# Kernel optimization log

Hardware: AMD Instinct MI355X
Metric: run time of the kernel (lower is better)

Reference implementation:

```python
import jax, jax.numpy as jnp
import numpy as np

B, N, C = 2048, 4096, 1024
UNITS, RANK = 4096, 512


def _orth(key, shape):
    a = jax.random.normal(key, shape, dtype=jnp.float32)
    q, r = jnp.linalg.qr(a if shape[0] >= shape[1] else a.T)
    q = q * jnp.sign(jnp.diagonal(r))[None, :]
    return q if shape[0] >= shape[1] else q.T


def setup_inputs() -> dict:
    key = jax.random.key(0)
    k1, k2, k3, k4, k5, k6 = jax.random.split(key, 6)
    inputs = jax.random.normal(k1, (B, N), dtype=jnp.float32)
    context = jax.random.normal(k2, (B, C), dtype=jnp.float32)
    U = _orth(k3, (N, RANK))
    V = _orth(k4, (UNITS, RANK))
    W = _orth(k5, (C, RANK))
    # SingularValueInitializer stand-in: positive values scaled like glorot singular values
    S = jnp.abs(jax.random.normal(k6, (RANK,), dtype=jnp.float32)) * jnp.sqrt(2.0 / (N + UNITS))
    bias = jnp.zeros((UNITS,), dtype=jnp.float32)
    return {"inputs": inputs, "context": context, "U": U, "S": S, "V": V, "W": W, "bias": bias}


def reference(inputs, context, U, S, V, W, bias):
    # s_b = S + context @ W  -> per-batch singular values [B, R]
    s = S[None, :] + context @ W
    # Original: kernel_b = U diag(s_b) V^T; out_b = x_b @ kernel_b.
    # Associativity: out = ((x @ U) * s) @ V^T  -- identical math, no [B,N,M] intermediate.
    xu = inputs @ U                      # [B, R]
    out = (xu * s) @ V.T                 # [B, UNITS]
    out = out + bias[None, :]
    return jax.nn.relu(out)
```

## Files before the change

### kernel.cpp

```cpp
#include <hip/hip_runtime.h>
#include <hip/hip_bf16.h>

typedef __attribute__((ext_vector_type(8))) __bf16 bf16x8;
typedef __attribute__((ext_vector_type(4))) float f32x4;
typedef __attribute__((ext_vector_type(8))) unsigned short ushort8;
typedef __attribute__((ext_vector_type(4))) unsigned short ushort4v;

__device__ __forceinline__ unsigned short f2bf(float f) {
  unsigned u = __builtin_bit_cast(unsigned, f);
  u += 0x7FFFu + ((u >> 16) & 1u);
  return (unsigned short)(u >> 16);
}

__device__ __forceinline__ void gload_lds16(const void* g, void* l) {
  __builtin_amdgcn_global_load_lds(
      (const __attribute__((address_space(1))) void*)g,
      (__attribute__((address_space(3))) void*)l, 16, 0, 0);
}

__device__ __forceinline__ void barrier_fence() {
  __builtin_amdgcn_s_barrier();
  asm volatile("" ::: "memory");
}

template <int N>
__device__ __forceinline__ void waitvm() {
  if constexpr (N == 0)      asm volatile("s_waitcnt vmcnt(0)" ::: "memory");
  else if constexpr (N == 8) asm volatile("s_waitcnt vmcnt(8)" ::: "memory");
}

__global__ __launch_bounds__(256) void prep_kernel(
    const float* __restrict__ U, unsigned short* __restrict__ Ut,
    const float* __restrict__ W, unsigned short* __restrict__ Wt,
    const float* __restrict__ V, unsigned short* __restrict__ Vb) {
  __shared__ float tile[32][33];
  const int b = blockIdx.x;
  const int tid = threadIdx.x;
  if (b < 2560) {
    const float* src;
    unsigned short* dst;
    int rows, cols, bx, by;
    if (b < 2048) {
      src = U; dst = Ut; rows = 4096; cols = 512;
      bx = (b & 15) * 32; by = (b >> 4) * 32;
    } else {
      int bb = b - 2048;
      src = W; dst = Wt; rows = 1024; cols = 512;
      bx = (bb & 15) * 32; by = (bb >> 4) * 32;
    }
    const int tx = tid & 31, ty = tid >> 5;
    for (int i = ty; i < 32; i += 8)
      tile[i][tx] = src[(size_t)(by + i) * cols + bx + tx];
    __syncthreads();
    for (int i = ty; i < 32; i += 8)
      dst[(size_t)(bx + i) * rows + by + tx] = f2bf(tile[tx][i]);
  } else {
    const size_t i = (size_t)(b - 2560) * 256 + tid;
    const float4* s4 = reinterpret_cast<const float4*>(V) + 2 * i;
    float4 a = s4[0], c = s4[1];
    ushort8 o;
    o[0] = f2bf(a.x); o[1] = f2bf(a.y); o[2] = f2bf(a.z); o[3] = f2bf(a.w);
    o[4] = f2bf(c.x); o[5] = f2bf(c.y); o[6] = f2bf(c.z); o[7] = f2bf(c.w);
    *(reinterpret_cast<ushort8*>(Vb) + i) = o;
  }
}

template <int FM, int FN, int EPI, int DEPTH>
__device__ __forceinline__ void gemm_core(
    const unsigned short* __restrict__ A, const unsigned short* __restrict__ Bt,
    int N, int lda, int kchunk, const float* __restrict__ e0,
    float* __restrict__ outf, int nwg, int bid) {
  constexpr int BM = 32 * FM, BN = 32 * FN, BK = 64;
  constexpr int AI = FM, BI = FN;
  constexpr int ISS = AI + BI;
  __shared__ unsigned short lds[DEPTH][(BM + BN) * BK];

  const int tid = threadIdx.x;
  const int wid = tid >> 6;
  const int lane = tid & 63;
  const int wr = wid >> 1, wc = wid & 1;

  const int swz = (bid & 7) * (nwg >> 3) + (bid >> 3);
  const int nbn = N / BN;
  const int brow = (swz / nbn) * BM;
  const int bcol = (swz % nbn) * BN;

  f32x4 zero = {0.f, 0.f, 0.f, 0.f};
  f32x4 acc[FM][FN];
#pragma unroll
  for (int m = 0; m < FM; ++m)
#pragma unroll
    for (int n = 0; n < FN; ++n) acc[m][n] = zero;

  const int lr = lane >> 3;
  const int swzc = ((lane & 7) ^ lr) * 8;
  const unsigned short* Agh = A + (size_t)(brow + wid * (BM / 4) + lr) * lda + swzc;
  const unsigned short* Bgh = Bt + (size_t)(bcol + wid * (BN / 4) + lr) * lda + swzc;

  const int frow = lane & 15;
  const int fhi = lane >> 4;

  const int nsteps = kchunk / BK;

  auto stage = [&](int b, int kofs) {
    unsigned short* AsW = lds[b] + wid * (BM / 4) * 64;
#pragma unroll
    for (int i = 0; i < AI; ++i)
      gload_lds16(Agh + kofs + (size_t)(8 * i) * lda, AsW + i * 512);
    unsigned short* BsW = lds[b] + BM * BK + wid * (BN / 4) * 64;
#pragma unroll
    for (int i = 0; i < BI; ++i)
      gload_lds16(Bgh + kofs + (size_t)(8 * i) * lda, BsW + i * 512);
  };

  auto compute = [&](int cur) {
    const unsigned short* As = lds[cur];
    const unsigned short* Bs = lds[cur] + BM * BK;
#pragma unroll
    for (int ks = 0; ks < 2; ++ks) {
      bf16x8 af[FM], bg[FN];
#pragma unroll
      for (int m = 0; m < FM; ++m) {
        int row = wr * FM * 16 + m * 16 + frow;
        int pc = (ks * 4 + fhi) ^ (row & 7);
        af[m] = *reinterpret_cast<const bf16x8*>(As + row * 64 + pc * 8);
      }
#pragma unroll
      for (int n = 0; n < FN; ++n) {
        int row = wc * FN * 16 + n * 16 + frow;
        int pc = (ks * 4 + fhi) ^ (row & 7);
        bg[n] = *reinterpret_cast<const bf16x8*>(Bs + row * 64 + pc * 8);
      }
#pragma unroll
      for (int m = 0; m < FM; ++m)
#pragma unroll
        for (int n = 0; n < FN; ++n)
          acc[m][n] = __builtin_amdgcn_mfma_f32_16x16x32_bf16(af[m], bg[n],
                                                              acc[m][n], 0, 0, 0);
    }
  };

#pragma unroll
  for (int d = 0; d < DEPTH; ++d) stage(d, d * BK);

  int cur = 0;
  for (int t = 0; t < nsteps; ++t) {
    const int ahead = nsteps - 1 - t;
    if (ahead >= DEPTH - 1)
      waitvm<(DEPTH - 1) * ISS>();
    else
      waitvm<0>();
    barrier_fence();
    compute(cur);
    if (t + 1 < nsteps) {
      asm volatile("s_waitcnt lgkmcnt(0)" ::: "memory");
      barrier_fence();
      if (t + DEPTH < nsteps) stage(cur, (t + DEPTH) * BK);
    }
    cur = (cur + 1 == DEPTH) ? 0 : cur + 1;
  }

#pragma unroll
  for (int m = 0; m < FM; ++m) {
    int gr0 = brow + wr * FM * 16 + m * 16 + fhi * 4;
#pragma unroll
    for (int n = 0; n < FN; ++n) {
      int gc = bcol + wc * FN * 16 + n * 16 + frow;
#pragma unroll
      for (int j = 0; j < 4; ++j) {
        size_t idx = (size_t)(gr0 + j) * N + gc;
        float v = acc[m][n][j];
        if constexpr (EPI == 2) {
          v += e0[gc];
          outf[idx] = v > 0.f ? v : 0.f;
        } else {
          outf[idx] = v;
        }
      }
    }
  }
}

__device__ __forceinline__ void gemm_core_f32a(
    const float* __restrict__ A, const unsigned short* __restrict__ Bt,
    int lda, int kchunk, float* __restrict__ outf, int nwg, int bid) {
  constexpr int N = 512;
  constexpr int BM = 128, BN = 128, BK = 64;
  __shared__ unsigned short lds[2][(BM + BN) * BK];

  const int tid = threadIdx.x;
  const int wid = tid >> 6;
  const int lane = tid & 63;
  const int wr = wid >> 1, wc = wid & 1;

  const int swz = (bid & 7) * (nwg >> 3) + (bid >> 3);
  const int nbn = N / BN;
  const int brow = (swz / nbn) * BM;
  const int bcol = (swz % nbn) * BN;

  f32x4 zero = {0.f, 0.f, 0.f, 0.f};
  f32x4 acc[4][4];
#pragma unroll
  for (int m = 0; m < 4; ++m)
#pragma unroll
    for (int n = 0; n < 4; ++n) acc[m][n] = zero;

  const int lr = lane >> 3;
  const int lc = lane & 7;
  const int swzc = (lc ^ lr) * 8;
  const float* Agf = A + (size_t)(brow + wid * 32 + lr) * lda + swzc;
  const unsigned short* Bgh = Bt + (size_t)(bcol + wid * 32 + lr) * lda + swzc;

  const int frow = lane & 15;
  const int fhi = lane >> 4;

  const int nsteps = kchunk / BK;

  float4 areg[4][2];
  auto aload = [&](int kofs) {
#pragma unroll
    for (int i = 0; i < 4; ++i) {
      const float* s = Agf + kofs + (size_t)(8 * i) * lda;
      areg[i][0] = *reinterpret_cast<const float4*>(s);
      areg[i][1] = *reinterpret_cast<const float4*>(s + 4);
    }
  };
  auto awrite = [&](int b) {
    unsigned short* AsW = lds[b] + wid * 2048 + lane * 8;
#pragma unroll
    for (int i = 0; i < 4; ++i) {
      float4 x = areg[i][0], y = areg[i][1];
      ushort8 o;
      o[0] = f2bf(x.x); o[1] = f2bf(x.y); o[2] = f2bf(x.z); o[3] = f2bf(x.w);
      o[4] = f2bf(y.x); o[5] = f2bf(y.y); o[6] = f2bf(y.z); o[7] = f2bf(y.w);
      *reinterpret_cast<ushort8*>(AsW + i * 512) = o;
    }
  };
  auto bload = [&](int b, int kofs) {
    unsigned short* BsW = lds[b] + BM * BK + wid * 2048;
#pragma unroll
    for (int i = 0; i < 4; ++i)
      gload_lds16(Bgh + kofs + (size_t)(8 * i) * lda, BsW + i * 512);
  };

  auto compute = [&](int cur) {
    const unsigned short* As = lds[cur];
    const unsigned short* Bs = lds[cur] + BM * BK;
#pragma unroll
    for (int ks = 0; ks < 2; ++ks) {
      bf16x8 af[4], bg[4];
#pragma unroll
      for (int m = 0; m < 4; ++m) {
        int row = wr * 64 + m * 16 + frow;
        int pc = (ks * 4 + fhi) ^ (row & 7);
        af[m] = *reinterpret_cast<const bf16x8*>(As + row * 64 + pc * 8);
      }
#pragma unroll
      for (int n = 0; n < 4; ++n) {
        int row = wc * 64 + n * 16 + frow;
        int pc = (ks * 4 + fhi) ^ (row & 7);
        bg[n] = *reinterpret_cast<const bf16x8*>(Bs + row * 64 + pc * 8);
      }
#pragma unroll
      for (int m = 0; m < 4; ++m)
#pragma unroll
        for (int n = 0; n < 4; ++n)
          acc[m][n] = __builtin_amdgcn_mfma_f32_16x16x32_bf16(af[m], bg[n],
                                                              acc[m][n], 0, 0, 0);
    }
  };

  aload(0);
  bload(0, 0);
  waitvm<0>();
  awrite(0);
  aload(BK);
  asm volatile("s_waitcnt lgkmcnt(0)" ::: "memory");
  barrier_fence();

  for (int t = 0; t < nsteps; ++t) {
    const int cur = t & 1;
    if (t + 1 < nsteps) bload(cur ^ 1, (t + 1) * BK);
    compute(cur);
    if (t + 1 < nsteps) {
      waitvm<0>();
      awrite(cur ^ 1);
      if (t + 2 < nsteps) aload((t + 2) * BK);
      asm volatile("s_waitcnt lgkmcnt(0)" ::: "memory");
      barrier_fence();
    }
  }

#pragma unroll
  for (int m = 0; m < 4; ++m) {
    int gr0 = brow + wr * 64 + m * 16 + fhi * 4;
#pragma unroll
    for (int n = 0; n < 4; ++n) {
      int gc = bcol + wc * 64 + n * 16 + frow;
#pragma unroll
      for (int j = 0; j < 4; ++j)
        outf[(size_t)(gr0 + j) * N + gc] = acc[m][n][j];
    }
  }
}

__global__ __launch_bounds__(256) void gemm01_kernel(
    const float* __restrict__ inp, const unsigned short* __restrict__ Ut,
    const float* __restrict__ ctx, const unsigned short* __restrict__ Wt,
    float* __restrict__ p0, float* __restrict__ p1) {
  const int bid = (int)blockIdx.x;
  constexpr size_t MN = (size_t)2048 * 512;
  if (bid < 256) {
    const int split = bid >> 6;
    gemm_core_f32a(inp + (size_t)split * 1024, Ut + (size_t)split * 1024,
                   4096, 1024, p1 + split * MN, 64, bid & 63);
  } else {
    const int sb = bid - 256;
    const int split = sb >> 6;
    gemm_core_f32a(ctx + (size_t)split * 512, Wt + (size_t)split * 512,
                   1024, 512, p0 + split * MN, 64, sb & 63);
  }
}

__global__ __launch_bounds__(256) void gemm2_kernel(
    const unsigned short* __restrict__ xus, const unsigned short* __restrict__ Vb,
    const float* __restrict__ bias, float* __restrict__ out) {
  gemm_core<4, 4, 2, 2>(xus, Vb, 4096, 512, 512, bias, out, 512,
                        (int)blockIdx.x);
}

__global__ void reduce_mul_kernel(const float* __restrict__ p1,
                                  const float* __restrict__ p0,
                                  const float* __restrict__ Svec,
                                  unsigned short* __restrict__ xus, int MN) {
  int i = blockIdx.x * blockDim.x + threadIdx.x;
  size_t base = (size_t)i * 4;
  if (base >= (size_t)MN) return;
  float4 a = *reinterpret_cast<const float4*>(p1 + base);
  float4 b = *reinterpret_cast<const float4*>(p1 + (size_t)MN + base);
  float4 c = *reinterpret_cast<const float4*>(p1 + 2 * (size_t)MN + base);
  float4 d = *reinterpret_cast<const float4*>(p1 + 3 * (size_t)MN + base);
  float4 s0 = *reinterpret_cast<const float4*>(p0 + base);
  float4 s1 = *reinterpret_cast<const float4*>(p0 + (size_t)MN + base);
  float4 sv = *reinterpret_cast<const float4*>(Svec + (base & 511));
  float4 xu, s;
  xu.x = (a.x + b.x) + (c.x + d.x);  s.x = s0.x + s1.x + sv.x;
  xu.y = (a.y + b.y) + (c.y + d.y);  s.y = s0.y + s1.y + sv.y;
  xu.z = (a.z + b.z) + (c.z + d.z);  s.z = s0.z + s1.z + sv.z;
  xu.w = (a.w + b.w) + (c.w + d.w);  s.w = s0.w + s1.w + sv.w;
  ushort4v o;
  o[0] = f2bf(xu.x * s.x);
  o[1] = f2bf(xu.y * s.y);
  o[2] = f2bf(xu.z * s.z);
  o[3] = f2bf(xu.w * s.w);
  *reinterpret_cast<ushort4v*>(xus + base) = o;
}

extern "C" void kernel_launch(void* const* d_in, const int* in_sizes, int n_in,
                              void* d_out, int out_size, void* d_ws, size_t ws_size,
                              hipStream_t stream) {
  constexpr int Bm = 2048, Nn = 4096, Cc = 1024, UU = 4096, RR = 512;
  const float* inputs  = (const float*)d_in[0];
  const float* context = (const float*)d_in[1];
  const float* U       = (const float*)d_in[2];
  const float* S       = (const float*)d_in[3];
  const float* V       = (const float*)d_in[4];
  const float* W       = (const float*)d_in[5];
  const float* bias    = (const float*)d_in[6];
  float* out = (float*)d_out;

  char* p = (char*)d_ws;
  unsigned short* Ut   = (unsigned short*)p; p += (size_t)RR * Nn * 2;
  unsigned short* Wt   = (unsigned short*)p; p += (size_t)RR * Cc * 2;
  unsigned short* Vb   = (unsigned short*)p; p += (size_t)UU * RR * 2;
  float*          p0   = (float*)p;          p += (size_t)2 * Bm * RR * 4;
  float*          p1   = (float*)p;          p += (size_t)4 * Bm * RR * 4;
  unsigned short* xus  = (unsigned short*)p; p += (size_t)Bm * RR * 2;

  prep_kernel<<<3584, 256, 0, stream>>>(U, Ut, W, Wt, V, Vb);

  gemm01_kernel<<<384, 256, 0, stream>>>(inputs, Ut, context, Wt, p0, p1);

  reduce_mul_kernel<<<Bm * RR / 4 / 256, 256, 0, stream>>>(p1, p0, S, xus, Bm * RR);

  gemm2_kernel<<<512, 256, 0, stream>>>(xus, Vb, bias, out);
}
```

Before: 52.10 us.

## Drop split-K for context GEMM, fuse S add, column-major tile order in gemm2

The context@W GEMM no longer uses split-K. It now runs as one 64-block pass over the full K=1024, and the S vector is added in its epilogue, so it writes a single s buffer instead of two partials. The reduce kernel then reads one float4 for s instead of two partials plus S, which cuts its memory traffic. The gemm2 tile mapping becomes column-major to change L2 reuse of the V operand versus the activations. The cost is fewer blocks in gemm01 (320 instead of 384), with the context blocks each running twice as long, which may unbalance the launch.

```diff
diff --git a/kernel.cpp b/kernel.cpp
--- a/kernel.cpp
+++ b/kernel.cpp
@@ -65,7 +65,7 @@
   }
 }
 
-template <int FM, int FN, int EPI, int DEPTH>
+template <int FM, int FN, int EPI, int DEPTH, bool COLMAP>
 __device__ __forceinline__ void gemm_core(
     const unsigned short* __restrict__ A, const unsigned short* __restrict__ Bt,
     int N, int lda, int kchunk, const float* __restrict__ e0,
@@ -82,8 +82,15 @@
 
   const int swz = (bid & 7) * (nwg >> 3) + (bid >> 3);
   const int nbn = N / BN;
-  const int brow = (swz / nbn) * BM;
-  const int bcol = (swz % nbn) * BN;
+  int brow, bcol;
+  if constexpr (COLMAP) {
+    const int nbm = nwg / nbn;
+    brow = (swz % nbm) * BM;
+    bcol = (swz / nbm) * BN;
+  } else {
+    brow = (swz / nbn) * BM;
+    bcol = (swz % nbn) * BN;
+  }
 
   f32x4 zero = {0.f, 0.f, 0.f, 0.f};
   f32x4 acc[FM][FN];
@@ -181,9 +188,11 @@
   }
 }
 
+template <int EPI>
 __device__ __forceinline__ void gemm_core_f32a(
     const float* __restrict__ A, const unsigned short* __restrict__ Bt,
-    int lda, int kchunk, float* __restrict__ outf, int nwg, int bid) {
+    int lda, int kchunk, const float* __restrict__ e0,
+    float* __restrict__ outf, int nwg, int bid) {
   constexpr int N = 512;
   constexpr int BM = 128, BN = 128, BK = 64;
   __shared__ unsigned short lds[2][(BM + BN) * BK];
@@ -298,8 +307,11 @@
     for (int n = 0; n < 4; ++n) {
       int gc = bcol + wc * 64 + n * 16 + frow;
 #pragma unroll
-      for (int j = 0; j < 4; ++j)
-        outf[(size_t)(gr0 + j) * N + gc] = acc[m][n][j];
+      for (int j = 0; j < 4; ++j) {
+        float v = acc[m][n][j];
+        if constexpr (EPI == 0) v += e0[gc];
+        outf[(size_t)(gr0 + j) * N + gc] = v;
+      }
     }
   }
 }
@@ -307,31 +319,28 @@
 __global__ __launch_bounds__(256) void gemm01_kernel(
     const float* __restrict__ inp, const unsigned short* __restrict__ Ut,
     const float* __restrict__ ctx, const unsigned short* __restrict__ Wt,
-    float* __restrict__ p0, float* __restrict__ p1) {
+    const float* __restrict__ S, float* __restrict__ sbuf,
+    float* __restrict__ p1) {
   const int bid = (int)blockIdx.x;
   constexpr size_t MN = (size_t)2048 * 512;
   if (bid < 256) {
     const int split = bid >> 6;
-    gemm_core_f32a(inp + (size_t)split * 1024, Ut + (size_t)split * 1024,
-                   4096, 1024, p1 + split * MN, 64, bid & 63);
+    gemm_core_f32a<3>(inp + (size_t)split * 1024, Ut + (size_t)split * 1024,
+                      4096, 1024, nullptr, p1 + split * MN, 64, bid & 63);
   } else {
-    const int sb = bid - 256;
-    const int split = sb >> 6;
-    gemm_core_f32a(ctx + (size_t)split * 512, Wt + (size_t)split * 512,
-                   1024, 512, p0 + split * MN, 64, sb & 63);
+    gemm_core_f32a<0>(ctx, Wt, 1024, 1024, S, sbuf, 64, bid - 256);
   }
 }
 
 __global__ __launch_bounds__(256) void gemm2_kernel(
     const unsigned short* __restrict__ xus, const unsigned short* __restrict__ Vb,
     const float* __restrict__ bias, float* __restrict__ out) {
-  gemm_core<4, 4, 2, 2>(xus, Vb, 4096, 512, 512, bias, out, 512,
-                        (int)blockIdx.x);
+  gemm_core<4, 4, 2, 2, true>(xus, Vb, 4096, 512, 512, bias, out, 512,
+                              (int)blockIdx.x);
 }
 
 __global__ void reduce_mul_kernel(const float* __restrict__ p1,
-                                  const float* __restrict__ p0,
-                                  const float* __restrict__ Svec,
+                                  const float* __restrict__ sbuf,
                                   unsigned short* __restrict__ xus, int MN) {
   int i = blockIdx.x * blockDim.x + threadIdx.x;
   size_t base = (size_t)i * 4;
@@ -340,14 +349,12 @@
   float4 b = *reinterpret_cast<const float4*>(p1 + (size_t)MN + base);
   float4 c = *reinterpret_cast<const float4*>(p1 + 2 * (size_t)MN + base);
   float4 d = *reinterpret_cast<const float4*>(p1 + 3 * (size_t)MN + base);
-  float4 s0 = *reinterpret_cast<const float4*>(p0 + base);
-  float4 s1 = *reinterpret_cast<const float4*>(p0 + (size_t)MN + base);
-  float4 sv = *reinterpret_cast<const float4*>(Svec + (base & 511));
-  float4 xu, s;
-  xu.x = (a.x + b.x) + (c.x + d.x);  s.x = s0.x + s1.x + sv.x;
-  xu.y = (a.y + b.y) + (c.y + d.y);  s.y = s0.y + s1.y + sv.y;
-  xu.z = (a.z + b.z) + (c.z + d.z);  s.z = s0.z + s1.z + sv.z;
-  xu.w = (a.w + b.w) + (c.w + d.w);  s.w = s0.w + s1.w + sv.w;
+  float4 s = *reinterpret_cast<const float4*>(sbuf + base);
+  float4 xu;
+  xu.x = (a.x + b.x) + (c.x + d.x);
+  xu.y = (a.y + b.y) + (c.y + d.y);
+  xu.z = (a.z + b.z) + (c.z + d.z);
+  xu.w = (a.w + b.w) + (c.w + d.w);
   ushort4v o;
   o[0] = f2bf(xu.x * s.x);
   o[1] = f2bf(xu.y * s.y);
@@ -373,15 +380,15 @@
   unsigned short* Ut   = (unsigned short*)p; p += (size_t)RR * Nn * 2;
   unsigned short* Wt   = (unsigned short*)p; p += (size_t)RR * Cc * 2;
   unsigned short* Vb   = (unsigned short*)p; p += (size_t)UU * RR * 2;
-  float*          p0   = (float*)p;          p += (size_t)2 * Bm * RR * 4;
+  float*          sbuf = (float*)p;          p += (size_t)Bm * RR * 4;
   float*          p1   = (float*)p;          p += (size_t)4 * Bm * RR * 4;
   unsigned short* xus  = (unsigned short*)p; p += (size_t)Bm * RR * 2;
 
   prep_kernel<<<3584, 256, 0, stream>>>(U, Ut, W, Wt, V, Vb);
 
-  gemm01_kernel<<<384, 256, 0, stream>>>(inputs, Ut, context, Wt, p0, p1);
-
-  reduce_mul_kernel<<<Bm * RR / 4 / 256, 256, 0, stream>>>(p1, p0, S, xus, Bm * RR);
+  gemm01_kernel<<<320, 256, 0, stream>>>(inputs, Ut, context, Wt, S, sbuf, p1);
+
+  reduce_mul_kernel<<<Bm * RR / 4 / 256, 256, 0, stream>>>(p1, sbuf, xus, Bm * RR);
 
   gemm2_kernel<<<512, 256, 0, stream>>>(xus, Vb, bias, out);
 }
```

Result: slower. 68.61 us (+31.7%).

## Double-buffer A/B register prefetch in fp32-A GEMM and column-major tile map

Applied to the files above, without the earlier changes.

The fp32-A GEMM used for x@U and ctx@W now loads both A and B tiles into two banks of registers two steps ahead, then writes them into LDS itself. Before, B went straight to LDS via global_load_lds and A was prefetched only one step ahead. This lets loads overlap two compute steps and drops the vmcnt waits inside the loop. The cost is more register pressure, and the loop now advances two K-steps per iteration, which assumes nsteps is even. The output GEMM switches to a column-major block mapping so that concurrent workgroups share V tiles, and the dispatcher is restructured into a single call site.

```diff
diff --git a/kernel.cpp b/kernel.cpp
--- a/kernel.cpp
+++ b/kernel.cpp
@@ -65,7 +65,7 @@
   }
 }
 
-template <int FM, int FN, int EPI, int DEPTH>
+template <int FM, int FN, int EPI, int DEPTH, bool COLMAP>
 __device__ __forceinline__ void gemm_core(
     const unsigned short* __restrict__ A, const unsigned short* __restrict__ Bt,
     int N, int lda, int kchunk, const float* __restrict__ e0,
@@ -82,8 +82,15 @@
 
   const int swz = (bid & 7) * (nwg >> 3) + (bid >> 3);
   const int nbn = N / BN;
-  const int brow = (swz / nbn) * BM;
-  const int bcol = (swz % nbn) * BN;
+  int brow, bcol;
+  if constexpr (COLMAP) {
+    const int nbm = nwg / nbn;
+    brow = (swz % nbm) * BM;
+    bcol = (swz / nbm) * BN;
+  } else {
+    brow = (swz / nbn) * BM;
+    bcol = (swz % nbn) * BN;
+  }
 
   f32x4 zero = {0.f, 0.f, 0.f, 0.f};
   f32x4 acc[FM][FN];
@@ -216,32 +223,38 @@
 
   const int nsteps = kchunk / BK;
 
-  float4 areg[4][2];
-  auto aload = [&](int kofs) {
-#pragma unroll
-    for (int i = 0; i < 4; ++i) {
-      const float* s = Agf + kofs + (size_t)(8 * i) * lda;
-      areg[i][0] = *reinterpret_cast<const float4*>(s);
-      areg[i][1] = *reinterpret_cast<const float4*>(s + 4);
-    }
-  };
-  auto awrite = [&](int b) {
-    unsigned short* AsW = lds[b] + wid * 2048 + lane * 8;
-#pragma unroll
-    for (int i = 0; i < 4; ++i) {
-      float4 x = areg[i][0], y = areg[i][1];
-      ushort8 o;
-      o[0] = f2bf(x.x); o[1] = f2bf(x.y); o[2] = f2bf(x.z); o[3] = f2bf(x.w);
-      o[4] = f2bf(y.x); o[5] = f2bf(y.y); o[6] = f2bf(y.z); o[7] = f2bf(y.w);
-      *reinterpret_cast<ushort8*>(AsW + i * 512) = o;
-    }
-  };
-  auto bload = [&](int b, int kofs) {
-    unsigned short* BsW = lds[b] + BM * BK + wid * 2048;
-#pragma unroll
-    for (int i = 0; i < 4; ++i)
-      gload_lds16(Bgh + kofs + (size_t)(8 * i) * lda, BsW + i * 512);
-  };
+  float4 areg0[4][2], areg1[4][2];
+  ushort8 breg0[4], breg1[4];
+
+#define ALOAD(bank, kofs)                                              \
+  _Pragma("unroll") for (int i = 0; i < 4; ++i) {                      \
+    const float* s_ = Agf + (kofs) + (size_t)(8 * i) * lda;            \
+    bank[i][0] = *reinterpret_cast<const float4*>(s_);                 \
+    bank[i][1] = *reinterpret_cast<const float4*>(s_ + 4);             \
+  }
+#define BLOAD(bank, kofs)                                              \
+  _Pragma("unroll") for (int i = 0; i < 4; ++i)                        \
+    bank[i] = *reinterpret_cast<const ushort8*>(Bgh + (kofs) +         \
+                                                (size_t)(8 * i) * lda);
+#define AWRITE(buf, bank)                                              \
+  {                                                                    \
+    unsigned short* AsW_ = lds[buf] + wid * 2048 + lane * 8;           \
+    _Pragma("unroll") for (int i = 0; i < 4; ++i) {                    \
+      float4 x_ = bank[i][0], y_ = bank[i][1];                         \
+      ushort8 o_;                                                      \
+      o_[0] = f2bf(x_.x); o_[1] = f2bf(x_.y);                          \
+      o_[2] = f2bf(x_.z); o_[3] = f2bf(x_.w);                          \
+      o_[4] = f2bf(y_.x); o_[5] = f2bf(y_.y);                          \
+      o_[6] = f2bf(y_.z); o_[7] = f2bf(y_.w);                          \
+      *reinterpret_cast<ushort8*>(AsW_ + i * 512) = o_;                \
+    }                                                                  \
+  }
+#define BWRITE(buf, bank)                                              \
+  {                                                                    \
+    unsigned short* BsW_ = lds[buf] + BM * BK + wid * 2048 + lane * 8; \
+    _Pragma("unroll") for (int i = 0; i < 4; ++i)                      \
+      *reinterpret_cast<ushort8*>(BsW_ + i * 512) = bank[i];           \
+  }
 
   auto compute = [&](int cur) {
     const unsigned short* As = lds[cur];
@@ -270,26 +283,31 @@
     }
   };
 
-  aload(0);
-  bload(0, 0);
-  waitvm<0>();
-  awrite(0);
-  aload(BK);
+  ALOAD(areg0, 0); BLOAD(breg0, 0);
+  ALOAD(areg1, BK); BLOAD(breg1, BK);
+  AWRITE(0, areg0); BWRITE(0, breg0);
   asm volatile("s_waitcnt lgkmcnt(0)" ::: "memory");
   barrier_fence();
 
-  for (int t = 0; t < nsteps; ++t) {
-    const int cur = t & 1;
-    if (t + 1 < nsteps) bload(cur ^ 1, (t + 1) * BK);
-    compute(cur);
-    if (t + 1 < nsteps) {
-      waitvm<0>();
-      awrite(cur ^ 1);
-      if (t + 2 < nsteps) aload((t + 2) * BK);
+  for (int t = 0; t < nsteps; t += 2) {
+    if (t + 2 < nsteps) { ALOAD(areg0, (t + 2) * BK); BLOAD(breg0, (t + 2) * BK); }
+    compute(0);
+    AWRITE(1, areg1); BWRITE(1, breg1);
+    asm volatile("s_waitcnt lgkmcnt(0)" ::: "memory");
+    barrier_fence();
+
+    if (t + 3 < nsteps) { ALOAD(areg1, (t + 3) * BK); BLOAD(breg1, (t + 3) * BK); }
+    compute(1);
+    if (t + 2 < nsteps) {
+      AWRITE(0, areg0); BWRITE(0, breg0);
       asm volatile("s_waitcnt lgkmcnt(0)" ::: "memory");
       barrier_fence();
     }
   }
+#undef ALOAD
+#undef BLOAD
+#undef AWRITE
+#undef BWRITE
 
 #pragma unroll
   for (int m = 0; m < 4; ++m) {
@@ -310,23 +328,30 @@
     float* __restrict__ p0, float* __restrict__ p1) {
   const int bid = (int)blockIdx.x;
   constexpr size_t MN = (size_t)2048 * 512;
+  const float* A;
+  const unsigned short* Bt;
+  int lda, kchunk, lbid;
+  float* outp;
   if (bid < 256) {
     const int split = bid >> 6;
-    gemm_core_f32a(inp + (size_t)split * 1024, Ut + (size_t)split * 1024,
-                   4096, 1024, p1 + split * MN, 64, bid & 63);
+    A = inp + (size_t)split * 1024;
+    Bt = Ut + (size_t)split * 1024;
+    lda = 4096; kchunk = 1024; outp = p1 + split * MN; lbid = bid & 63;
   } else {
     const int sb = bid - 256;
     const int split = sb >> 6;
-    gemm_core_f32a(ctx + (size_t)split * 512, Wt + (size_t)split * 512,
-                   1024, 512, p0 + split * MN, 64, sb & 63);
-  }
+    A = ctx + (size_t)split * 512;
+    Bt = Wt + (size_t)split * 512;
+    lda = 1024; kchunk = 512; outp = p0 + split * MN; lbid = sb & 63;
+  }
+  gemm_core_f32a(A, Bt, lda, kchunk, outp, 64, lbid);
 }
 
 __global__ __launch_bounds__(256) void gemm2_kernel(
     const unsigned short* __restrict__ xus, const unsigned short* __restrict__ Vb,
     const float* __restrict__ bias, float* __restrict__ out) {
-  gemm_core<4, 4, 2, 2>(xus, Vb, 4096, 512, 512, bias, out, 512,
-                        (int)blockIdx.x);
+  gemm_core<4, 4, 2, 2, true>(xus, Vb, 4096, 512, 512, bias, out, 512,
+                              (int)blockIdx.x);
 }
 
 __global__ void reduce_mul_kernel(const float* __restrict__ p1,
```

After: 60.45 us. 1.16x slower.
